# Kernel optimization log

Measured on AMD Instinct MI355X. Metric: run time of the kernel, lower is better.

Reference implementation:

```python
import jax, jax.numpy as jnp
import numpy as np

N_NODES = 100000
IN_DIM = 128
N_EDGES = 600000
HIDDEN = 128


def setup_inputs() -> dict:
    key = jax.random.key(0)
    k_z, k_e, k_w1, k_b1, k_w2, k_b2 = jax.random.split(key, 6)
    z = jax.random.normal(k_z, (N_NODES, IN_DIM), dtype=jnp.float32)
    edge_index = jax.random.randint(k_e, (2, N_EDGES), 0, N_NODES, dtype=jnp.int64)
    # torch.nn.Linear weights: W has shape (out, in), y = x @ W.T + b
    lim1 = 1.0 / np.sqrt(2 * IN_DIM)
    W1 = jax.random.uniform(k_w1, (HIDDEN, 2 * IN_DIM), jnp.float32, -lim1, lim1)
    b1 = jax.random.uniform(k_b1, (HIDDEN,), jnp.float32, -lim1, lim1)
    lim2 = 1.0 / np.sqrt(HIDDEN)
    W2 = jax.random.uniform(k_w2, (1, HIDDEN), jnp.float32, -lim2, lim2)
    b2 = jax.random.uniform(k_b2, (1,), jnp.float32, -lim2, lim2)
    return {"z": z, "edge_index": edge_index, "W1": W1, "b1": b1, "W2": W2, "b2": b2}


def reference(z, edge_index, W1, b1, W2, b2):
    src, dst = edge_index[0], edge_index[1]
    pair = jnp.concatenate([z[src], z[dst]], axis=1)        # [E, 2*in_dim]
    h = jax.nn.relu(pair @ W1.T + b1)                        # [E, 128]
    out = (h @ W2.T + b2).squeeze(-1)                        # [E]
    return out
```

## Files before the change

### kernel.cpp

```cpp
#include <hip/hip_runtime.h>

#define IN_DIM 128
#define NCOL   256
#define TPITCH (NCOL + 8)

typedef __bf16 bfx8 __attribute__((ext_vector_type(8)));
typedef __bf16 bfx4 __attribute__((ext_vector_type(4)));
typedef float  f32x4 __attribute__((ext_vector_type(4)));

__global__ __launch_bounds__(256) void prep_w(
    const float* __restrict__ W1, __bf16* __restrict__ Weff)
{
    const int n = threadIdx.x;
    const float* src = (n < 128) ? (W1 + n * 256) : (W1 + (n - 128) * 256 + 128);
    __bf16* dst = Weff + n * IN_DIM;
#pragma unroll
    for (int k = 0; k < IN_DIM; k += 4) {
        float4 f = *(const float4*)(src + k);
        bfx4 b;
        b[0] = (__bf16)f.x; b[1] = (__bf16)f.y; b[2] = (__bf16)f.z; b[3] = (__bf16)f.w;
        *(bfx4*)(dst + k) = b;
    }
}

__global__ __launch_bounds__(256) void gemm_mfma(
    const float* __restrict__ z, const __bf16* __restrict__ Weff,
    const float* __restrict__ b1, __bf16* __restrict__ UV, int M)
{
    __shared__ __bf16 tile[32][TPITCH];

    const int tid  = threadIdx.x;
    const int wave = tid >> 6;
    const int lane = tid & 63;
    const int l15  = lane & 15;
    const int q    = lane >> 4;
    const int n0   = wave * 64;

    bfx8  bfrag[4][4];
    float bias[4];
#pragma unroll
    for (int nt = 0; nt < 4; ++nt) {
        const int n = n0 + nt * 16 + l15;
        bias[nt] = (n < 128) ? b1[n] : 0.f;
#pragma unroll
        for (int kk = 0; kk < 4; ++kk)
            bfrag[nt][kk] = *(const bfx8*)(Weff + n * IN_DIM + kk * 32 + q * 8);
    }

    const int mbeg = blockIdx.x * 64;
    const int mend = (mbeg + 64 < M) ? (mbeg + 64) : M;

    for (int m0 = mbeg; m0 < mend; m0 += 32) {
        bfx8 afrag[2][4];
#pragma unroll
        for (int mt = 0; mt < 2; ++mt) {
#pragma unroll
            for (int kk = 0; kk < 4; ++kk) {
                const float* p = z + (size_t)(m0 + mt * 16 + l15) * IN_DIM + kk * 32 + q * 8;
                float4 f0 = *(const float4*)p;
                float4 f1 = *(const float4*)(p + 4);
                bfx8 a;
                a[0] = (__bf16)f0.x; a[1] = (__bf16)f0.y; a[2] = (__bf16)f0.z; a[3] = (__bf16)f0.w;
                a[4] = (__bf16)f1.x; a[5] = (__bf16)f1.y; a[6] = (__bf16)f1.z; a[7] = (__bf16)f1.w;
                afrag[mt][kk] = a;
            }
        }

        f32x4 acc[2][4];
#pragma unroll
        for (int mt = 0; mt < 2; ++mt)
#pragma unroll
            for (int nt = 0; nt < 4; ++nt)
                acc[mt][nt] = (f32x4){0.f, 0.f, 0.f, 0.f};

#pragma unroll
        for (int kk = 0; kk < 4; ++kk)
#pragma unroll
            for (int mt = 0; mt < 2; ++mt)
#pragma unroll
                for (int nt = 0; nt < 4; ++nt)
                    acc[mt][nt] = __builtin_amdgcn_mfma_f32_16x16x32_bf16(
                        afrag[mt][kk], bfrag[nt][kk], acc[mt][nt], 0, 0, 0);

#pragma unroll
        for (int mt = 0; mt < 2; ++mt)
#pragma unroll
            for (int nt = 0; nt < 4; ++nt) {
                const int col = n0 + nt * 16 + l15;
#pragma unroll
                for (int r = 0; r < 4; ++r)
                    tile[mt * 16 + q * 4 + r][col] = (__bf16)(acc[mt][nt][r] + bias[nt]);
            }
        __syncthreads();

#pragma unroll
        for (int s = 0; s < 4; ++s) {
            const int lin = s * 256 + tid;
            const int row = lin >> 5;
            const int c   = lin & 31;
            bfx8 v = *(const bfx8*)&tile[row][c * 8];
            *(bfx8*)(UV + (size_t)(m0 + row) * NCOL + c * 8) = v;
        }
        __syncthreads();
    }
}

__global__ __launch_bounds__(256) void edge_mlp(
    const __bf16* __restrict__ UV, const int* __restrict__ ei,
    const float* __restrict__ W2, const float* __restrict__ b2,
    float* __restrict__ out, int E)
{
    const int gt   = blockIdx.x * blockDim.x + threadIdx.x;
    const int lane = threadIdx.x & 15;
    const int g    = gt >> 4;
    const int e0   = g * 2;
    const int j0   = lane * 8;

    float ww[8];
    {
        float4 w0 = *(const float4*)(W2 + j0);
        float4 w1 = *(const float4*)(W2 + j0 + 4);
        ww[0] = w0.x; ww[1] = w0.y; ww[2] = w0.z; ww[3] = w0.w;
        ww[4] = w1.x; ww[5] = w1.y; ww[6] = w1.z; ww[7] = w1.w;
    }

    if (e0 >= E) return;

    const int2 srcp = *(const int2*)(ei + e0);
    const int2 dstp = *(const int2*)(ei + E + e0);

    bfx8 u0 = *(const bfx8*)(UV + (size_t)srcp.x * NCOL + j0);
    bfx8 v0 = *(const bfx8*)(UV + (size_t)dstp.x * NCOL + 128 + j0);
    bfx8 u1 = *(const bfx8*)(UV + (size_t)srcp.y * NCOL + j0);
    bfx8 v1 = *(const bfx8*)(UV + (size_t)dstp.y * NCOL + 128 + j0);

    float s0 = 0.f, s1 = 0.f;
#pragma unroll
    for (int i = 0; i < 8; ++i) {
        float h0 = (float)u0[i] + (float)v0[i];
        float h1 = (float)u1[i] + (float)v1[i];
        s0 = fmaf(fmaxf(h0, 0.f), ww[i], s0);
        s1 = fmaf(fmaxf(h1, 0.f), ww[i], s1);
    }

#pragma unroll
    for (int d = 1; d < 16; d <<= 1) {
        s0 += __shfl_xor(s0, d);
        s1 += __shfl_xor(s1, d);
    }

    if (lane == 0) {
        float bb = b2[0];
        *(float2*)(out + e0) = make_float2(s0 + bb, s1 + bb);
    }
}

extern "C" void kernel_launch(void* const* d_in, const int* in_sizes, int n_in,
                              void* d_out, int out_size, void* d_ws, size_t ws_size,
                              hipStream_t stream)
{
    const float* z  = (const float*)d_in[0];
    const int*   ei = (const int*)d_in[1];
    const float* W1 = (const float*)d_in[2];
    const float* b1 = (const float*)d_in[3];
    const float* W2 = (const float*)d_in[4];
    const float* b2 = (const float*)d_in[5];
    float* out = (float*)d_out;

    const int M = in_sizes[0] / IN_DIM;
    const int E = in_sizes[1] / 2;

    __bf16* UV   = (__bf16*)d_ws;
    __bf16* Weff = UV + (size_t)M * NCOL;

    prep_w<<<1, 256, 0, stream>>>(W1, Weff);

    int gblocks = (M + 63) / 64;
    gemm_mfma<<<gblocks, 256, 0, stream>>>(z, Weff, b1, UV, M);

    int groups  = (E + 1) / 2;
    int eblocks = (groups * 16 + 255) / 256;
    edge_mlp<<<eblocks, 256, 0, stream>>>(UV, ei, W2, b2, out, E);
}
```

Baseline: 175.6 us.

## Fuse W1 bf16 conversion into GEMM, one tile per block, 4 edges per group

Removes the separate prep_w launch: each GEMM block now reads W1 in fp32 and converts it to bf16 fragments itself. The GEMM handles one 32-row tile per block instead of looping over two, doubling the block count. The edge kernel processes four edges per 16-lane group with int4 index loads and float4 stores, giving more gathers in flight per thread. This saves a launch and its serialization, but each block now re-reads and converts W1, and the edge path assumes E is a multiple of 4 and M a multiple of 32.

```diff
diff --git a/kernel.cpp b/kernel.cpp
--- a/kernel.cpp
+++ b/kernel.cpp
@@ -5,26 +5,10 @@
 #define TPITCH (NCOL + 8)
 
 typedef __bf16 bfx8 __attribute__((ext_vector_type(8)));
-typedef __bf16 bfx4 __attribute__((ext_vector_type(4)));
 typedef float  f32x4 __attribute__((ext_vector_type(4)));
 
-__global__ __launch_bounds__(256) void prep_w(
-    const float* __restrict__ W1, __bf16* __restrict__ Weff)
-{
-    const int n = threadIdx.x;
-    const float* src = (n < 128) ? (W1 + n * 256) : (W1 + (n - 128) * 256 + 128);
-    __bf16* dst = Weff + n * IN_DIM;
-#pragma unroll
-    for (int k = 0; k < IN_DIM; k += 4) {
-        float4 f = *(const float4*)(src + k);
-        bfx4 b;
-        b[0] = (__bf16)f.x; b[1] = (__bf16)f.y; b[2] = (__bf16)f.z; b[3] = (__bf16)f.w;
-        *(bfx4*)(dst + k) = b;
-    }
-}
-
 __global__ __launch_bounds__(256) void gemm_mfma(
-    const float* __restrict__ z, const __bf16* __restrict__ Weff,
+    const float* __restrict__ z, const float* __restrict__ W1,
     const float* __restrict__ b1, __bf16* __restrict__ UV, int M)
 {
     __shared__ __bf16 tile[32][TPITCH];
@@ -35,6 +19,22 @@
     const int l15  = lane & 15;
     const int q    = lane >> 4;
     const int n0   = wave * 64;
+    const int m0   = blockIdx.x * 32;
+
+    bfx8 afrag[2][4];
+#pragma unroll
+    for (int mt = 0; mt < 2; ++mt) {
+#pragma unroll
+        for (int kk = 0; kk < 4; ++kk) {
+            const float* p = z + (size_t)(m0 + mt * 16 + l15) * IN_DIM + kk * 32 + q * 8;
+            float4 f0 = *(const float4*)p;
+            float4 f1 = *(const float4*)(p + 4);
+            bfx8 a;
+            a[0] = (__bf16)f0.x; a[1] = (__bf16)f0.y; a[2] = (__bf16)f0.z; a[3] = (__bf16)f0.w;
+            a[4] = (__bf16)f1.x; a[5] = (__bf16)f1.y; a[6] = (__bf16)f1.z; a[7] = (__bf16)f1.w;
+            afrag[mt][kk] = a;
+        }
+    }
 
     bfx8  bfrag[4][4];
     float bias[4];
@@ -43,65 +43,53 @@
         const int n = n0 + nt * 16 + l15;
         bias[nt] = (n < 128) ? b1[n] : 0.f;
 #pragma unroll
-        for (int kk = 0; kk < 4; ++kk)
-            bfrag[nt][kk] = *(const bfx8*)(Weff + n * IN_DIM + kk * 32 + q * 8);
+        for (int kk = 0; kk < 4; ++kk) {
+            const int k = kk * 32 + q * 8;
+            const float* p = (n < 128) ? (W1 + n * 256 + k)
+                                       : (W1 + (n - 128) * 256 + 128 + k);
+            float4 f0 = *(const float4*)p;
+            float4 f1 = *(const float4*)(p + 4);
+            bfx8 b;
+            b[0] = (__bf16)f0.x; b[1] = (__bf16)f0.y; b[2] = (__bf16)f0.z; b[3] = (__bf16)f0.w;
+            b[4] = (__bf16)f1.x; b[5] = (__bf16)f1.y; b[6] = (__bf16)f1.z; b[7] = (__bf16)f1.w;
+            bfrag[nt][kk] = b;
+        }
     }
 
-    const int mbeg = blockIdx.x * 64;
-    const int mend = (mbeg + 64 < M) ? (mbeg + 64) : M;
+    f32x4 acc[2][4];
+#pragma unroll
+    for (int mt = 0; mt < 2; ++mt)
+#pragma unroll
+        for (int nt = 0; nt < 4; ++nt)
+            acc[mt][nt] = (f32x4){0.f, 0.f, 0.f, 0.f};
 
-    for (int m0 = mbeg; m0 < mend; m0 += 32) {
-        bfx8 afrag[2][4];
 #pragma unroll
-        for (int mt = 0; mt < 2; ++mt) {
-#pragma unroll
-            for (int kk = 0; kk < 4; ++kk) {
-                const float* p = z + (size_t)(m0 + mt * 16 + l15) * IN_DIM + kk * 32 + q * 8;
-                float4 f0 = *(const float4*)p;
-                float4 f1 = *(const float4*)(p + 4);
-                bfx8 a;
-                a[0] = (__bf16)f0.x; a[1] = (__bf16)f0.y; a[2] = (__bf16)f0.z; a[3] = (__bf16)f0.w;
-                a[4] = (__bf16)f1.x; a[5] = (__bf16)f1.y; a[6] = (__bf16)f1.z; a[7] = (__bf16)f1.w;
-                afrag[mt][kk] = a;
-            }
-        }
-
-        f32x4 acc[2][4];
+    for (int kk = 0; kk < 4; ++kk)
 #pragma unroll
         for (int mt = 0; mt < 2; ++mt)
 #pragma unroll
             for (int nt = 0; nt < 4; ++nt)
-                acc[mt][nt] = (f32x4){0.f, 0.f, 0.f, 0.f};
+                acc[mt][nt] = __builtin_amdgcn_mfma_f32_16x16x32_bf16(
+                    afrag[mt][kk], bfrag[nt][kk], acc[mt][nt], 0, 0, 0);
 
 #pragma unroll
-        for (int kk = 0; kk < 4; ++kk)
+    for (int mt = 0; mt < 2; ++mt)
 #pragma unroll
-            for (int mt = 0; mt < 2; ++mt)
+        for (int nt = 0; nt < 4; ++nt) {
+            const int col = n0 + nt * 16 + l15;
 #pragma unroll
-                for (int nt = 0; nt < 4; ++nt)
-                    acc[mt][nt] = __builtin_amdgcn_mfma_f32_16x16x32_bf16(
-                        afrag[mt][kk], bfrag[nt][kk], acc[mt][nt], 0, 0, 0);
+            for (int r = 0; r < 4; ++r)
+                tile[mt * 16 + q * 4 + r][col] = (__bf16)(acc[mt][nt][r] + bias[nt]);
+        }
+    __syncthreads();
 
 #pragma unroll
-        for (int mt = 0; mt < 2; ++mt)
-#pragma unroll
-            for (int nt = 0; nt < 4; ++nt) {
-                const int col = n0 + nt * 16 + l15;
-#pragma unroll
-                for (int r = 0; r < 4; ++r)
-                    tile[mt * 16 + q * 4 + r][col] = (__bf16)(acc[mt][nt][r] + bias[nt]);
-            }
-        __syncthreads();
-
-#pragma unroll
-        for (int s = 0; s < 4; ++s) {
-            const int lin = s * 256 + tid;
-            const int row = lin >> 5;
-            const int c   = lin & 31;
-            bfx8 v = *(const bfx8*)&tile[row][c * 8];
-            *(bfx8*)(UV + (size_t)(m0 + row) * NCOL + c * 8) = v;
-        }
-        __syncthreads();
+    for (int s = 0; s < 4; ++s) {
+        const int lin = s * 256 + tid;
+        const int row = lin >> 5;
+        const int c   = lin & 31;
+        bfx8 v = *(const bfx8*)&tile[row][c * 8];
+        *(bfx8*)(UV + (size_t)(m0 + row) * NCOL + c * 8) = v;
     }
 }
 
@@ -113,7 +101,7 @@
     const int gt   = blockIdx.x * blockDim.x + threadIdx.x;
     const int lane = threadIdx.x & 15;
     const int g    = gt >> 4;
-    const int e0   = g * 2;
+    const int e0   = g * 4;
     const int j0   = lane * 8;
 
     float ww[8];
@@ -126,32 +114,38 @@
 
     if (e0 >= E) return;
 
-    const int2 srcp = *(const int2*)(ei + e0);
-    const int2 dstp = *(const int2*)(ei + E + e0);
+    const int4 s4 = *(const int4*)(ei + e0);
+    const int4 d4 = *(const int4*)(ei + E + e0);
 
-    bfx8 u0 = *(const bfx8*)(UV + (size_t)srcp.x * NCOL + j0);
-    bfx8 v0 = *(const bfx8*)(UV + (size_t)dstp.x * NCOL + 128 + j0);
-    bfx8 u1 = *(const bfx8*)(UV + (size_t)srcp.y * NCOL + j0);
-    bfx8 v1 = *(const bfx8*)(UV + (size_t)dstp.y * NCOL + 128 + j0);
+    bfx8 u0 = *(const bfx8*)(UV + (size_t)s4.x * NCOL + j0);
+    bfx8 u1 = *(const bfx8*)(UV + (size_t)s4.y * NCOL + j0);
+    bfx8 u2 = *(const bfx8*)(UV + (size_t)s4.z * NCOL + j0);
+    bfx8 u3 = *(const bfx8*)(UV + (size_t)s4.w * NCOL + j0);
+    bfx8 v0 = *(const bfx8*)(UV + (size_t)d4.x * NCOL + 128 + j0);
+    bfx8 v1 = *(const bfx8*)(UV + (size_t)d4.y * NCOL + 128 + j0);
+    bfx8 v2 = *(const bfx8*)(UV + (size_t)d4.z * NCOL + 128 + j0);
+    bfx8 v3 = *(const bfx8*)(UV + (size_t)d4.w * NCOL + 128 + j0);
 
-    float s0 = 0.f, s1 = 0.f;
+    float s0 = 0.f, s1 = 0.f, s2 = 0.f, s3 = 0.f;
 #pragma unroll
     for (int i = 0; i < 8; ++i) {
-        float h0 = (float)u0[i] + (float)v0[i];
-        float h1 = (float)u1[i] + (float)v1[i];
-        s0 = fmaf(fmaxf(h0, 0.f), ww[i], s0);
-        s1 = fmaf(fmaxf(h1, 0.f), ww[i], s1);
+        s0 = fmaf(fmaxf((float)u0[i] + (float)v0[i], 0.f), ww[i], s0);
+        s1 = fmaf(fmaxf((float)u1[i] + (float)v1[i], 0.f), ww[i], s1);
+        s2 = fmaf(fmaxf((float)u2[i] + (float)v2[i], 0.f), ww[i], s2);
+        s3 = fmaf(fmaxf((float)u3[i] + (float)v3[i], 0.f), ww[i], s3);
     }
 
 #pragma unroll
     for (int d = 1; d < 16; d <<= 1) {
         s0 += __shfl_xor(s0, d);
         s1 += __shfl_xor(s1, d);
+        s2 += __shfl_xor(s2, d);
+        s3 += __shfl_xor(s3, d);
     }
 
     if (lane == 0) {
-        float bb = b2[0];
-        *(float2*)(out + e0) = make_float2(s0 + bb, s1 + bb);
+        const float bb = b2[0];
+        *(float4*)(out + e0) = make_float4(s0 + bb, s1 + bb, s2 + bb, s3 + bb);
     }
 }
 
@@ -170,15 +164,11 @@
     const int M = in_sizes[0] / IN_DIM;
     const int E = in_sizes[1] / 2;
 
-    __bf16* UV   = (__bf16*)d_ws;
-    __bf16* Weff = UV + (size_t)M * NCOL;
+    __bf16* UV = (__bf16*)d_ws;
 
-    prep_w<<<1, 256, 0, stream>>>(W1, Weff);
+    gemm_mfma<<<M / 32, 256, 0, stream>>>(z, W1, b1, UV, M);
 
-    int gblocks = (M + 63) / 64;
-    gemm_mfma<<<gblocks, 256, 0, stream>>>(z, Weff, b1, UV, M);
-
-    int groups  = (E + 1) / 2;
-    int eblocks = (groups * 16 + 255) / 256;
+    const int groups  = (E + 3) / 4;
+    const int eblocks = (groups * 16 + 255) / 256;
     edge_mlp<<<eblocks, 256, 0, stream>>>(UV, ei, W2, b2, out, E);
 }
```

Result: slower. 197.2 us (+12.3%).
